# Kernel optimization log

Hardware: AMD Instinct MI355X
Metric: run time of the kernel (lower is better)

The kernel has to match this reference:

```python
import jax, jax.numpy as jnp
import numpy as np

EMB = 1024
HEADS = 16
HEAD_DIM = EMB // HEADS


def setup_inputs() -> dict:
    key = jax.random.key(0)
    k1, k2, k3, k4 = jax.random.split(key, 4)
    x = jax.random.normal(k1, (4, 2048, EMB), dtype=jnp.float32)
    # torch Linear weight is [out, in]; store as [in, out] for x @ W
    W_qkv = jax.random.normal(k2, (EMB, 3 * EMB), dtype=jnp.float32) * (1.0 / np.sqrt(EMB))
    W_proj = jax.random.normal(k3, (EMB, EMB), dtype=jnp.float32) * (1.0 / np.sqrt(EMB))
    b_proj = jax.random.normal(k4, (EMB,), dtype=jnp.float32) * 0.01
    return {"x": x, "W_qkv": W_qkv, "W_proj": W_proj, "b_proj": b_proj}


def reference(x, W_qkv, W_proj, b_proj):
    B, S, D = x.shape
    H, hd = HEADS, HEAD_DIM
    qkv = x @ W_qkv                                  # [B,S,3D]
    q, k, v = jnp.split(qkv, 3, axis=-1)
    q = q.reshape(B, S, H, hd).transpose(0, 2, 1, 3)  # [B,H,S,hd]
    k = k.reshape(B, S, H, hd).transpose(0, 2, 1, 3)
    v = v.reshape(B, S, H, hd).transpose(0, 2, 1, 3)
    att = jnp.einsum('bhqd,bhkd->bhqk', q, k) * (1.0 / np.sqrt(hd))
    causal = jnp.tril(jnp.ones((S, S), dtype=bool))
    att = jnp.where(causal[None, None], att, jnp.float32(-jnp.inf))
    att = jax.nn.softmax(att, axis=-1)
    # dropout omitted (eval mode / deterministic baseline)
    out = jnp.einsum('bhqk,bhkd->bhqd', att, v)       # [B,H,S,hd]
    out = out.transpose(0, 2, 1, 3).reshape(B, S, D)
    return out @ W_proj + b_proj
```

## Files before the change

kernel.cpp:

```cpp
#include <hip/hip_runtime.h>
#include <math.h>

#define S_   2048
#define D_   1024
#define H_   16
#define HD_  64
#define BH_  64
#define TOK_ 8192

typedef __attribute__((ext_vector_type(8))) short  short8;
typedef __attribute__((ext_vector_type(4))) float  floatx4;

__device__ __forceinline__ short f2bf(float f) {
  union { float f; unsigned u; } c; c.f = f;
  unsigned u = c.u;
  u += 0x7fffu + ((u >> 16) & 1u);
  return (short)(u >> 16);
}

__device__ __forceinline__ void gload16(const void* g, void* l) {
  __builtin_amdgcn_global_load_lds((const __attribute__((address_space(1))) void*)g,
                                   (__attribute__((address_space(3))) void*)l, 16, 0, 0);
}

__global__ void cvt_x_kernel(const float* __restrict__ in, short* __restrict__ out, int n8) {
  int i = blockIdx.x * blockDim.x + threadIdx.x;
  if (i >= n8) return;
  const float4* p = (const float4*)in;
  float4 a = p[i * 2], b = p[i * 2 + 1];
  short8 o;
  o[0] = f2bf(a.x); o[1] = f2bf(a.y); o[2] = f2bf(a.z); o[3] = f2bf(a.w);
  o[4] = f2bf(b.x); o[5] = f2bf(b.y); o[6] = f2bf(b.z); o[7] = f2bf(b.w);
  ((short8*)out)[i] = o;
}

__global__ void tconv_kernel(const float* __restrict__ in, short* __restrict__ out, int R, int C) {
  __shared__ float t[32][33];
  int tx = threadIdx.x, ty = threadIdx.y;
  int c0 = blockIdx.x * 32, r0 = blockIdx.y * 32;
#pragma unroll
  for (int i = 0; i < 4; ++i)
    t[ty + i * 8][tx] = in[(r0 + ty + i * 8) * C + c0 + tx];
  __syncthreads();
#pragma unroll
  for (int i = 0; i < 4; ++i)
    out[(c0 + ty + i * 8) * R + r0 + tx] = f2bf(t[tx][ty + i * 8]);
}

__global__ void tv_kernel(const short* __restrict__ vb, short* __restrict__ vtb) {
  __shared__ short t[32][33];
  int tx = threadIdx.x, ty = threadIdx.y;
  int bh = blockIdx.z;
  int d0 = blockIdx.x * 32, s0 = blockIdx.y * 32;
  const short* src = vb + bh * S_ * HD_;
  short* dst = vtb + bh * HD_ * S_;
#pragma unroll
  for (int i = 0; i < 4; ++i)
    t[ty + i * 8][tx] = src[(s0 + ty + i * 8) * HD_ + d0 + tx];
  __syncthreads();
#pragma unroll
  for (int i = 0; i < 4; ++i)
    dst[(d0 + ty + i * 8) * S_ + s0 + tx] = t[tx][ty + i * 8];
}

__global__ __launch_bounds__(256) void gemm_qkv_kernel(
    const short* __restrict__ A, const short* __restrict__ Bt,
    short* __restrict__ qb, short* __restrict__ kb, short* __restrict__ vb) {
  __shared__ short sA[128 * 32];
  __shared__ short sB[128 * 32];
  const int tid = threadIdx.x;
  const int lane = tid & 63, wid = tid >> 6;
  const int wm = wid >> 1, wn = wid & 1;
  const int lr = lane & 15, lg = lane >> 4;
  const int m0 = blockIdx.x * 128, n0 = blockIdx.y * 128;
  floatx4 acc[4][4] = {};
  const int f1 = tid * 16;
  const int rS1 = f1 >> 6, cS1 = (f1 & 63) >> 1;
  const int f2 = f1 + 4096;
  const int rS2 = f2 >> 6, cS2 = (f2 & 63) >> 1;
  for (int kt = 0; kt < 32; ++kt) {
    const int k0 = kt * 32;
    __syncthreads();
    gload16(&A[(m0 + rS1) * 1024 + k0 + cS1], (char*)sA + f1);
    gload16(&A[(m0 + rS2) * 1024 + k0 + cS2], (char*)sA + f2);
    gload16(&Bt[(n0 + rS1) * 1024 + k0 + cS1], (char*)sB + f1);
    gload16(&Bt[(n0 + rS2) * 1024 + k0 + cS2], (char*)sB + f2);
    __syncthreads();
    short8 af[4], bfv[4];
#pragma unroll
    for (int mf = 0; mf < 4; ++mf)
      af[mf] = *(const short8*)&sA[(wm * 64 + mf * 16 + lr) * 32 + lg * 8];
#pragma unroll
    for (int nf = 0; nf < 4; ++nf)
      bfv[nf] = *(const short8*)&sB[(wn * 64 + nf * 16 + lr) * 32 + lg * 8];
#pragma unroll
    for (int mf = 0; mf < 4; ++mf)
#pragma unroll
      for (int nf = 0; nf < 4; ++nf)
        acc[mf][nf] = __builtin_amdgcn_mfma_f32_16x16x32_bf16(af[mf], bfv[nf], acc[mf][nf], 0, 0, 0);
  }
  const int sec = n0 >> 10;
  short* dst = sec == 0 ? qb : (sec == 1 ? kb : vb);
  const float scale = (sec == 0) ? 0.125f : 1.0f;
#pragma unroll
  for (int mf = 0; mf < 4; ++mf) {
#pragma unroll
    for (int nf = 0; nf < 4; ++nf) {
      const int col = n0 + wn * 64 + nf * 16 + lr;
      const int w = col & 1023;
      const int h = w >> 6, d = w & 63;
#pragma unroll
      for (int r = 0; r < 4; ++r) {
        const int token = m0 + wm * 64 + mf * 16 + lg * 4 + r;
        const int b = token >> 11, s = token & 2047;
        dst[(((b << 4) | h) * 2048 + s) * 64 + d] = f2bf(acc[mf][nf][r] * scale);
      }
    }
  }
}

__global__ __launch_bounds__(256) void gemm_proj_kernel(
    const short* __restrict__ A, const short* __restrict__ Bt,
    const float* __restrict__ bias, float* __restrict__ out) {
  __shared__ short sA[128 * 32];
  __shared__ short sB[128 * 32];
  const int tid = threadIdx.x;
  const int lane = tid & 63, wid = tid >> 6;
  const int wm = wid >> 1, wn = wid & 1;
  const int lr = lane & 15, lg = lane >> 4;
  const int m0 = blockIdx.x * 128, n0 = blockIdx.y * 128;
  floatx4 acc[4][4] = {};
  const int f1 = tid * 16;
  const int rS1 = f1 >> 6, cS1 = (f1 & 63) >> 1;
  const int f2 = f1 + 4096;
  const int rS2 = f2 >> 6, cS2 = (f2 & 63) >> 1;
  for (int kt = 0; kt < 32; ++kt) {
    const int k0 = kt * 32;
    __syncthreads();
    gload16(&A[(m0 + rS1) * 1024 + k0 + cS1], (char*)sA + f1);
    gload16(&A[(m0 + rS2) * 1024 + k0 + cS2], (char*)sA + f2);
    gload16(&Bt[(n0 + rS1) * 1024 + k0 + cS1], (char*)sB + f1);
    gload16(&Bt[(n0 + rS2) * 1024 + k0 + cS2], (char*)sB + f2);
    __syncthreads();
    short8 af[4], bfv[4];
#pragma unroll
    for (int mf = 0; mf < 4; ++mf)
      af[mf] = *(const short8*)&sA[(wm * 64 + mf * 16 + lr) * 32 + lg * 8];
#pragma unroll
    for (int nf = 0; nf < 4; ++nf)
      bfv[nf] = *(const short8*)&sB[(wn * 64 + nf * 16 + lr) * 32 + lg * 8];
#pragma unroll
    for (int mf = 0; mf < 4; ++mf)
#pragma unroll
      for (int nf = 0; nf < 4; ++nf)
        acc[mf][nf] = __builtin_amdgcn_mfma_f32_16x16x32_bf16(af[mf], bfv[nf], acc[mf][nf], 0, 0, 0);
  }
#pragma unroll
  for (int mf = 0; mf < 4; ++mf) {
#pragma unroll
    for (int nf = 0; nf < 4; ++nf) {
      const int col = n0 + wn * 64 + nf * 16 + lr;
      const float bv = bias[col];
#pragma unroll
      for (int r = 0; r < 4; ++r) {
        const int row = m0 + wm * 64 + mf * 16 + lg * 4 + r;
        out[row * 1024 + col] = acc[mf][nf][r] + bv;
      }
    }
  }
}

__global__ __launch_bounds__(256) void attn_kernel(
    const short* __restrict__ qb, const short* __restrict__ kb,
    const short* __restrict__ vtb, short* __restrict__ attb) {
  __shared__ short sK[2][64 * 64];
  __shared__ short sVT[2][64 * 64];
  __shared__ short sP[4][32 * 64];
  const int tid = threadIdx.x;
  const int lane = tid & 63, wid = tid >> 6;
  const int lr = lane & 15, lg = lane >> 4;

  const int bid = blockIdx.x;
  const int wgid = (bid & 7) * 64 + (bid >> 3);
  const int bh = wgid >> 3;
  const int qx = wgid & 7;

  const char* kbase = (const char*)(kb + bh * S_ * HD_);
  const char* vtbase = (const char*)(vtb + bh * HD_ * S_);
  const short* qbase = qb + bh * S_ * HD_;
  char* pbase = (char*)&sP[wid][0];
  const int b = bh >> 4, h = bh & 15;

  const int f1 = tid * 16;
  const int ro1 = f1 >> 7, cb1 = f1 & 127;
  const int sc1 = cb1 ^ ((ro1 & 7) << 4);
  const int f2 = f1 + 4096;
  const int ro2 = f2 >> 7, cb2 = f2 & 127;
  const int sc2 = cb2 ^ ((ro2 & 7) << 4);

#pragma unroll 1
  for (int half = 0; half < 2; ++half) {
    const int qt = half ? (15 - qx) : qx;
    const int qw = qt * 128 + wid * 32;

    short8 qf[2][2];
#pragma unroll
    for (int mf = 0; mf < 2; ++mf)
#pragma unroll
      for (int kf = 0; kf < 2; ++kf)
        qf[mf][kf] = *(const short8*)&qbase[(qw + mf * 16 + lr) * 64 + kf * 32 + lg * 8];

    floatx4 acc_o[2][4] = {};
    float mrun[8], lrun[8];
#pragma unroll
    for (int i = 0; i < 8; ++i) { mrun[i] = -1e30f; lrun[i] = 0.f; }

    const int ntiles = 2 * qt + 2;

    {
      char* dK = (char*)sK[0];
      char* dV = (char*)sVT[0];
      gload16(kbase + ro1 * 128 + sc1, dK + f1);
      gload16(kbase + ro2 * 128 + sc2, dK + f2);
      gload16(vtbase + ro1 * 4096 + sc1, dV + f1);
      gload16(vtbase + ro2 * 4096 + sc2, dV + f2);
      asm volatile("s_waitcnt vmcnt(0)" ::: "memory");
      __builtin_amdgcn_s_barrier();
      __builtin_amdgcn_sched_barrier(0);
    }

    int cur = 0;
#pragma unroll 1
    for (int t = 0; t < ntiles; ++t) {
      if (t + 1 < ntiles) {
        const int key0n = (t + 1) * 64;
        char* dK = (char*)sK[cur ^ 1];
        char* dV = (char*)sVT[cur ^ 1];
        gload16(kbase + (key0n + ro1) * 128 + sc1, dK + f1);
        gload16(kbase + (key0n + ro2) * 128 + sc2, dK + f2);
        gload16(vtbase + ro1 * 4096 + key0n * 2 + sc1, dV + f1);
        gload16(vtbase + ro2 * 4096 + key0n * 2 + sc2, dV + f2);
      }
      const int key0 = t * 64;
      const char* cK = (const char*)sK[cur];
      const char* cV = (const char*)sVT[cur];

      floatx4 s_acc[2][4] = {};
      __builtin_amdgcn_s_setprio(1);
#pragma unroll
      for (int nf = 0; nf < 4; ++nf) {
#pragma unroll
        for (int kf = 0; kf < 2; ++kf) {
          const int row = nf * 16 + lr;
          const int cb = kf * 64 + lg * 16;
          short8 kfrag = *(const short8*)(cK + row * 128 + (cb ^ ((row & 7) << 4)));
#pragma unroll
          for (int mf = 0; mf < 2; ++mf)
            s_acc[mf][nf] = __builtin_amdgcn_mfma_f32_16x16x32_bf16(qf[mf][kf], kfrag, s_acc[mf][nf], 0, 0, 0);
        }
      }
      __builtin_amdgcn_s_setprio(0);

      const bool needmask = (key0 + 63 > qw);
#pragma unroll
      for (int mf = 0; mf < 2; ++mf) {
#pragma unroll
        for (int r = 0; r < 4; ++r) {
          const int qrow = qw + mf * 16 + lg * 4 + r;
          float sv[4];
          float mx = -1e30f;
#pragma unroll
          for (int nf = 0; nf < 4; ++nf) {
            float s = s_acc[mf][nf][r];
            if (needmask && (key0 + nf * 16 + lr > qrow)) s = -1e30f;
            sv[nf] = s;
            mx = fmaxf(mx, s);
          }
#pragma unroll
          for (int m = 1; m < 16; m <<= 1) mx = fmaxf(mx, __shfl_xor(mx, m));
          const int ri = mf * 4 + r;
          const float mnew = fmaxf(mrun[ri], mx);
          const float al = __expf(mrun[ri] - mnew);
          mrun[ri] = mnew;
          float ls = 0.f;
          const int qlocal = mf * 16 + lg * 4 + r;
          const int sw = (qlocal & 7) << 4;
#pragma unroll
          for (int nf = 0; nf < 4; ++nf) {
            float p = __expf(sv[nf] - mnew);
            ls += p;
            const int keyc = nf * 16 + lr;
            *(short*)(pbase + qlocal * 128 + ((keyc * 2) ^ sw)) = f2bf(p);
          }
#pragma unroll
          for (int m = 1; m < 16; m <<= 1) ls += __shfl_xor(ls, m);
          lrun[ri] = lrun[ri] * al + ls;
#pragma unroll
          for (int nfd = 0; nfd < 4; ++nfd) acc_o[mf][nfd][r] *= al;
        }
      }

      __builtin_amdgcn_s_setprio(1);
#pragma unroll
      for (int kf2 = 0; kf2 < 2; ++kf2) {
        short8 pf2[2];
#pragma unroll
        for (int mf = 0; mf < 2; ++mf) {
          const int rowp = mf * 16 + lr;
          const int cbp = kf2 * 64 + lg * 16;
          pf2[mf] = *(const short8*)(pbase + rowp * 128 + (cbp ^ ((rowp & 7) << 4)));
        }
#pragma unroll
        for (int nfd = 0; nfd < 4; ++nfd) {
          const int rowv = nfd * 16 + lr;
          const int cbv = kf2 * 64 + lg * 16;
          short8 vfrag = *(const short8*)(cV + rowv * 128 + (cbv ^ ((rowv & 7) << 4)));
#pragma unroll
          for (int mf = 0; mf < 2; ++mf)
            acc_o[mf][nfd] = __builtin_amdgcn_mfma_f32_16x16x32_bf16(pf2[mf], vfrag, acc_o[mf][nfd], 0, 0, 0);
        }
      }
      __builtin_amdgcn_s_setprio(0);

      __builtin_amdgcn_sched_barrier(0);
      asm volatile("s_waitcnt vmcnt(0)" ::: "memory");
      __builtin_amdgcn_s_barrier();
      __builtin_amdgcn_sched_barrier(0);
      cur ^= 1;
    }

#pragma unroll
    for (int mf = 0; mf < 2; ++mf) {
#pragma unroll
      for (int nfd = 0; nfd < 4; ++nfd) {
#pragma unroll
        for (int r = 0; r < 4; ++r) {
          const int ri = mf * 4 + r;
          const float o = acc_o[mf][nfd][r] / lrun[ri];
          const int qrow = qw + mf * 16 + lg * 4 + r;
          const int d = nfd * 16 + lr;
          attb[(b * 2048 + qrow) * 1024 + h * 64 + d] = f2bf(o);
        }
      }
    }
  }
}

extern "C" void kernel_launch(void* const* d_in, const int* in_sizes, int n_in,
                              void* d_out, int out_size, void* d_ws, size_t ws_size,
                              hipStream_t stream) {
  (void)in_sizes; (void)n_in; (void)out_size; (void)ws_size;
  const float* x = (const float*)d_in[0];
  const float* Wqkv = (const float*)d_in[1];
  const float* Wproj = (const float*)d_in[2];
  const float* bproj = (const float*)d_in[3];
  float* out = (float*)d_out;

  char* w = (char*)d_ws;
  short* xb     = (short*)(w + 0);
  short* wqkvT  = (short*)(w + 16777216);
  short* wprojT = (short*)(w + 23068672);
  short* qb     = (short*)(w + 25165824);
  short* kb     = (short*)(w + 41943040);
  short* vb     = (short*)(w + 58720256);
  short* vtb    = (short*)(w + 75497472);
  short* attb   = (short*)(w + 92274688);

  cvt_x_kernel<<<4096, 256, 0, stream>>>(x, xb, TOK_ * D_ / 8);
  tconv_kernel<<<dim3(96, 32), dim3(32, 8), 0, stream>>>(Wqkv, wqkvT, 1024, 3072);
  tconv_kernel<<<dim3(32, 32), dim3(32, 8), 0, stream>>>(Wproj, wprojT, 1024, 1024);
  gemm_qkv_kernel<<<dim3(64, 24), 256, 0, stream>>>(xb, wqkvT, qb, kb, vb);
  tv_kernel<<<dim3(2, 64, 64), dim3(32, 8), 0, stream>>>(vb, vtb);
  attn_kernel<<<512, 256, 0, stream>>>(qb, kb, vtb, attb);
  gemm_proj_kernel<<<dim3(64, 8), 256, 0, stream>>>(attb, wprojT, bproj, out);
}
```

Before: 316.2 us.

## Shrink attention query tiles and use lazy exp2 rescaling with MFMA row sums

Each block now covers a 64-row query tile instead of 128 rows, with 16 rows per wave, and the grid doubles to 1024 blocks for better parallelism and finer causal load balance. Softmax uses exp2 with log2(e) folded into the Q scale. The running max is only refreshed when some row's new max exceeds the old one by more than 8. The denominator is accumulated by an MFMA against a vector of ones instead of shuffle reductions. In exchange, K/V tiles are reloaded twice as often per query, and the lazy rescale lets unnormalized probabilities grow up to 2^8 before the final division.

```diff
diff --git a/kernel.cpp b/kernel.cpp
--- a/kernel.cpp
+++ b/kernel.cpp
@@ -101,7 +101,7 @@
   }
   const int sec = n0 >> 10;
   short* dst = sec == 0 ? qb : (sec == 1 ? kb : vb);
-  const float scale = (sec == 0) ? 0.125f : 1.0f;
+  const float scale = (sec == 0) ? 0.18033688011112042f : 1.0f;
 #pragma unroll
   for (int mf = 0; mf < 4; ++mf) {
 #pragma unroll
@@ -175,15 +175,15 @@
     const short* __restrict__ vtb, short* __restrict__ attb) {
   __shared__ short sK[2][64 * 64];
   __shared__ short sVT[2][64 * 64];
-  __shared__ short sP[4][32 * 64];
+  __shared__ short sP[4][16 * 64];
   const int tid = threadIdx.x;
   const int lane = tid & 63, wid = tid >> 6;
   const int lr = lane & 15, lg = lane >> 4;
 
   const int bid = blockIdx.x;
-  const int wgid = (bid & 7) * 64 + (bid >> 3);
-  const int bh = wgid >> 3;
-  const int qx = wgid & 7;
+  const int wgid = (bid & 7) * 128 + (bid >> 3);
+  const int bh = wgid >> 4;
+  const int qx = wgid & 15;
 
   const char* kbase = (const char*)(kb + bh * S_ * HD_);
   const char* vtbase = (const char*)(vtb + bh * HD_ * S_);
@@ -198,24 +198,27 @@
   const int ro2 = f2 >> 7, cb2 = f2 & 127;
   const int sc2 = cb2 ^ ((ro2 & 7) << 4);
 
+  short8 vones;
+#pragma unroll
+  for (int j = 0; j < 8; ++j) vones[j] = (short)0x3F80;
+
 #pragma unroll 1
   for (int half = 0; half < 2; ++half) {
-    const int qt = half ? (15 - qx) : qx;
-    const int qw = qt * 128 + wid * 32;
-
-    short8 qf[2][2];
-#pragma unroll
-    for (int mf = 0; mf < 2; ++mf)
-#pragma unroll
-      for (int kf = 0; kf < 2; ++kf)
-        qf[mf][kf] = *(const short8*)&qbase[(qw + mf * 16 + lr) * 64 + kf * 32 + lg * 8];
-
-    floatx4 acc_o[2][4] = {};
-    float mrun[8], lrun[8];
-#pragma unroll
-    for (int i = 0; i < 8; ++i) { mrun[i] = -1e30f; lrun[i] = 0.f; }
-
-    const int ntiles = 2 * qt + 2;
+    const int qt = half ? (31 - qx) : qx;
+    const int qw = qt * 64 + wid * 16;
+
+    short8 qf[2];
+#pragma unroll
+    for (int kf = 0; kf < 2; ++kf)
+      qf[kf] = *(const short8*)&qbase[(qw + lr) * 64 + kf * 32 + lg * 8];
+
+    floatx4 acc_o[4] = {};
+    floatx4 acc_den = {};
+    float mrun[4];
+#pragma unroll
+    for (int i = 0; i < 4; ++i) mrun[i] = -1e30f;
+
+    const int ntiles = qt + 1;
 
     {
       char* dK = (char*)sK[0];
@@ -245,7 +248,7 @@
       const char* cK = (const char*)sK[cur];
       const char* cV = (const char*)sVT[cur];
 
-      floatx4 s_acc[2][4] = {};
+      floatx4 s_acc[4] = {};
       __builtin_amdgcn_s_setprio(1);
 #pragma unroll
       for (int nf = 0; nf < 4; ++nf) {
@@ -254,70 +257,63 @@
           const int row = nf * 16 + lr;
           const int cb = kf * 64 + lg * 16;
           short8 kfrag = *(const short8*)(cK + row * 128 + (cb ^ ((row & 7) << 4)));
-#pragma unroll
-          for (int mf = 0; mf < 2; ++mf)
-            s_acc[mf][nf] = __builtin_amdgcn_mfma_f32_16x16x32_bf16(qf[mf][kf], kfrag, s_acc[mf][nf], 0, 0, 0);
+          s_acc[nf] = __builtin_amdgcn_mfma_f32_16x16x32_bf16(qf[kf], kfrag, s_acc[nf], 0, 0, 0);
         }
       }
       __builtin_amdgcn_s_setprio(0);
 
       const bool needmask = (key0 + 63 > qw);
-#pragma unroll
-      for (int mf = 0; mf < 2; ++mf) {
+      float mx[4];
+      bool need = false;
+#pragma unroll
+      for (int r = 0; r < 4; ++r) {
+        const int qrow = qw + lg * 4 + r;
+        if (needmask) {
+#pragma unroll
+          for (int nf = 0; nf < 4; ++nf)
+            if (key0 + nf * 16 + lr > qrow) s_acc[nf][r] = -1e30f;
+        }
+        float m01 = fmaxf(s_acc[0][r], s_acc[1][r]);
+        float m23 = fmaxf(s_acc[2][r], s_acc[3][r]);
+        float mxl = fmaxf(m01, m23);
+#pragma unroll
+        for (int m = 1; m < 16; m <<= 1) mxl = fmaxf(mxl, __shfl_xor(mxl, m));
+        mx[r] = mxl;
+        need = need || (mxl > mrun[r] + 8.f);
+      }
+      if (__any(need)) {
 #pragma unroll
         for (int r = 0; r < 4; ++r) {
-          const int qrow = qw + mf * 16 + lg * 4 + r;
-          float sv[4];
-          float mx = -1e30f;
-#pragma unroll
-          for (int nf = 0; nf < 4; ++nf) {
-            float s = s_acc[mf][nf][r];
-            if (needmask && (key0 + nf * 16 + lr > qrow)) s = -1e30f;
-            sv[nf] = s;
-            mx = fmaxf(mx, s);
-          }
-#pragma unroll
-          for (int m = 1; m < 16; m <<= 1) mx = fmaxf(mx, __shfl_xor(mx, m));
-          const int ri = mf * 4 + r;
-          const float mnew = fmaxf(mrun[ri], mx);
-          const float al = __expf(mrun[ri] - mnew);
-          mrun[ri] = mnew;
-          float ls = 0.f;
-          const int qlocal = mf * 16 + lg * 4 + r;
-          const int sw = (qlocal & 7) << 4;
-#pragma unroll
-          for (int nf = 0; nf < 4; ++nf) {
-            float p = __expf(sv[nf] - mnew);
-            ls += p;
-            const int keyc = nf * 16 + lr;
-            *(short*)(pbase + qlocal * 128 + ((keyc * 2) ^ sw)) = f2bf(p);
-          }
-#pragma unroll
-          for (int m = 1; m < 16; m <<= 1) ls += __shfl_xor(ls, m);
-          lrun[ri] = lrun[ri] * al + ls;
-#pragma unroll
-          for (int nfd = 0; nfd < 4; ++nfd) acc_o[mf][nfd][r] *= al;
+          const float mnew = fmaxf(mrun[r], mx[r]);
+          const float al = exp2f(mrun[r] - mnew);
+          mrun[r] = mnew;
+          acc_den[r] *= al;
+#pragma unroll
+          for (int nfd = 0; nfd < 4; ++nfd) acc_o[nfd][r] *= al;
+        }
+      }
+#pragma unroll
+      for (int r = 0; r < 4; ++r) {
+        const int qlocal = lg * 4 + r;
+        const int sw = (qlocal & 7) << 4;
+#pragma unroll
+        for (int nf = 0; nf < 4; ++nf) {
+          const float p = exp2f(s_acc[nf][r] - mrun[r]);
+          *(short*)(pbase + qlocal * 128 + ((nf * 32 + lr * 2) ^ sw)) = f2bf(p);
         }
       }
 
       __builtin_amdgcn_s_setprio(1);
 #pragma unroll
       for (int kf2 = 0; kf2 < 2; ++kf2) {
-        short8 pf2[2];
-#pragma unroll
-        for (int mf = 0; mf < 2; ++mf) {
-          const int rowp = mf * 16 + lr;
-          const int cbp = kf2 * 64 + lg * 16;
-          pf2[mf] = *(const short8*)(pbase + rowp * 128 + (cbp ^ ((rowp & 7) << 4)));
-        }
+        const short8 pf = *(const short8*)(pbase + lr * 128 + ((kf2 * 64 + lg * 16) ^ ((lr & 7) << 4)));
+        acc_den = __builtin_amdgcn_mfma_f32_16x16x32_bf16(pf, vones, acc_den, 0, 0, 0);
 #pragma unroll
         for (int nfd = 0; nfd < 4; ++nfd) {
           const int rowv = nfd * 16 + lr;
           const int cbv = kf2 * 64 + lg * 16;
           short8 vfrag = *(const short8*)(cV + rowv * 128 + (cbv ^ ((rowv & 7) << 4)));
-#pragma unroll
-          for (int mf = 0; mf < 2; ++mf)
-            acc_o[mf][nfd] = __builtin_amdgcn_mfma_f32_16x16x32_bf16(pf2[mf], vfrag, acc_o[mf][nfd], 0, 0, 0);
+          acc_o[nfd] = __builtin_amdgcn_mfma_f32_16x16x32_bf16(pf, vfrag, acc_o[nfd], 0, 0, 0);
         }
       }
       __builtin_amdgcn_s_setprio(0);
@@ -330,17 +326,13 @@
     }
 
 #pragma unroll
-    for (int mf = 0; mf < 2; ++mf) {
-#pragma unroll
-      for (int nfd = 0; nfd < 4; ++nfd) {
-#pragma unroll
-        for (int r = 0; r < 4; ++r) {
-          const int ri = mf * 4 + r;
-          const float o = acc_o[mf][nfd][r] / lrun[ri];
-          const int qrow = qw + mf * 16 + lg * 4 + r;
-          const int d = nfd * 16 + lr;
-          attb[(b * 2048 + qrow) * 1024 + h * 64 + d] = f2bf(o);
-        }
+    for (int nfd = 0; nfd < 4; ++nfd) {
+#pragma unroll
+      for (int r = 0; r < 4; ++r) {
+        const float o = acc_o[nfd][r] / acc_den[r];
+        const int qrow = qw + lg * 4 + r;
+        const int d = nfd * 16 + lr;
+        attb[(b * 2048 + qrow) * 1024 + h * 64 + d] = f2bf(o);
       }
     }
   }
@@ -371,6 +363,6 @@
   tconv_kernel<<<dim3(32, 32), dim3(32, 8), 0, stream>>>(Wproj, wprojT, 1024, 1024);
   gemm_qkv_kernel<<<dim3(64, 24), 256, 0, stream>>>(xb, wqkvT, qb, kb, vb);
   tv_kernel<<<dim3(2, 64, 64), dim3(32, 8), 0, stream>>>(vb, vtb);
-  attn_kernel<<<512, 256, 0, stream>>>(qb, kb, vtb, attb);
+  attn_kernel<<<1024, 256, 0, stream>>>(qb, kb, vtb, attb);
   gemm_proj_kernel<<<dim3(64, 8), 256, 0, stream>>>(attb, wprojT, bproj, out);
 }
```

New measurement: 327.2 us. 1.03x slower.

## Restructure flash-attention softmax with transposed scores, lazy rescale, and MFMA row sums

Applied to the files above, without the earlier changes.

Computes S transposed (K·Q) so each lane holds one query column, which cuts the max reduction to two cross-lane shuffles. Folds log2(e) into the Q scale so exp2 can replace expf, and rescales only when a row max grows by more than 8 (a lazy threshold). Computes the softmax denominator with an extra MFMA against a ones vector, packs P with v_cvt_pk_bf16 into 64-bit LDS stores, and skips key tiles that lie fully above the causal diagonal for a warp. In exchange it adds two MFMAs per tile, and the lazy max carries a numerical risk because unnormalized values can reach up to 2^8.

```diff
diff --git a/kernel.cpp b/kernel.cpp
--- a/kernel.cpp
+++ b/kernel.cpp
@@ -101,7 +101,7 @@
   }
   const int sec = n0 >> 10;
   short* dst = sec == 0 ? qb : (sec == 1 ? kb : vb);
-  const float scale = (sec == 0) ? 0.125f : 1.0f;
+  const float scale = (sec == 0) ? 0.18033688011112042f : 1.0f;
 #pragma unroll
   for (int mf = 0; mf < 4; ++mf) {
 #pragma unroll
@@ -198,6 +198,12 @@
   const int ro2 = f2 >> 7, cb2 = f2 & 127;
   const int sc2 = cb2 ^ ((ro2 & 7) << 4);
 
+  const int swz = (lr & 7) << 4;
+
+  short8 vones;
+#pragma unroll
+  for (int j = 0; j < 8; ++j) vones[j] = (short)0x3F80;
+
 #pragma unroll 1
   for (int half = 0; half < 2; ++half) {
     const int qt = half ? (15 - qx) : qx;
@@ -205,15 +211,14 @@
 
     short8 qf[2][2];
 #pragma unroll
-    for (int mf = 0; mf < 2; ++mf)
+    for (int qtile = 0; qtile < 2; ++qtile)
 #pragma unroll
       for (int kf = 0; kf < 2; ++kf)
-        qf[mf][kf] = *(const short8*)&qbase[(qw + mf * 16 + lr) * 64 + kf * 32 + lg * 8];
+        qf[qtile][kf] = *(const short8*)&qbase[(qw + qtile * 16 + lr) * 64 + kf * 32 + lg * 8];
 
     floatx4 acc_o[2][4] = {};
-    float mrun[8], lrun[8];
-#pragma unroll
-    for (int i = 0; i < 8; ++i) { mrun[i] = -1e30f; lrun[i] = 0.f; }
+    floatx4 acc_den[2] = {};
+    float mrun[2] = {-1e30f, -1e30f};
 
     const int ntiles = 2 * qt + 2;
 
@@ -242,85 +247,102 @@
         gload16(vtbase + ro2 * 4096 + key0n * 2 + sc2, dV + f2);
       }
       const int key0 = t * 64;
-      const char* cK = (const char*)sK[cur];
-      const char* cV = (const char*)sVT[cur];
-
-      floatx4 s_acc[2][4] = {};
-      __builtin_amdgcn_s_setprio(1);
-#pragma unroll
-      for (int nf = 0; nf < 4; ++nf) {
-#pragma unroll
-        for (int kf = 0; kf < 2; ++kf) {
-          const int row = nf * 16 + lr;
-          const int cb = kf * 64 + lg * 16;
-          short8 kfrag = *(const short8*)(cK + row * 128 + (cb ^ ((row & 7) << 4)));
-#pragma unroll
-          for (int mf = 0; mf < 2; ++mf)
-            s_acc[mf][nf] = __builtin_amdgcn_mfma_f32_16x16x32_bf16(qf[mf][kf], kfrag, s_acc[mf][nf], 0, 0, 0);
-        }
-      }
-      __builtin_amdgcn_s_setprio(0);
-
-      const bool needmask = (key0 + 63 > qw);
-#pragma unroll
-      for (int mf = 0; mf < 2; ++mf) {
-#pragma unroll
-        for (int r = 0; r < 4; ++r) {
-          const int qrow = qw + mf * 16 + lg * 4 + r;
-          float sv[4];
-          float mx = -1e30f;
-#pragma unroll
-          for (int nf = 0; nf < 4; ++nf) {
-            float s = s_acc[mf][nf][r];
-            if (needmask && (key0 + nf * 16 + lr > qrow)) s = -1e30f;
-            sv[nf] = s;
-            mx = fmaxf(mx, s);
-          }
-#pragma unroll
-          for (int m = 1; m < 16; m <<= 1) mx = fmaxf(mx, __shfl_xor(mx, m));
-          const int ri = mf * 4 + r;
-          const float mnew = fmaxf(mrun[ri], mx);
-          const float al = __expf(mrun[ri] - mnew);
-          mrun[ri] = mnew;
-          float ls = 0.f;
-          const int qlocal = mf * 16 + lg * 4 + r;
-          const int sw = (qlocal & 7) << 4;
-#pragma unroll
-          for (int nf = 0; nf < 4; ++nf) {
-            float p = __expf(sv[nf] - mnew);
-            ls += p;
-            const int keyc = nf * 16 + lr;
-            *(short*)(pbase + qlocal * 128 + ((keyc * 2) ^ sw)) = f2bf(p);
-          }
-#pragma unroll
-          for (int m = 1; m < 16; m <<= 1) ls += __shfl_xor(ls, m);
-          lrun[ri] = lrun[ri] * al + ls;
-#pragma unroll
-          for (int nfd = 0; nfd < 4; ++nfd) acc_o[mf][nfd][r] *= al;
-        }
-      }
-
-      __builtin_amdgcn_s_setprio(1);
-#pragma unroll
-      for (int kf2 = 0; kf2 < 2; ++kf2) {
-        short8 pf2[2];
-#pragma unroll
-        for (int mf = 0; mf < 2; ++mf) {
-          const int rowp = mf * 16 + lr;
-          const int cbp = kf2 * 64 + lg * 16;
-          pf2[mf] = *(const short8*)(pbase + rowp * 128 + (cbp ^ ((rowp & 7) << 4)));
-        }
-#pragma unroll
-        for (int nfd = 0; nfd < 4; ++nfd) {
-          const int rowv = nfd * 16 + lr;
-          const int cbv = kf2 * 64 + lg * 16;
-          short8 vfrag = *(const short8*)(cV + rowv * 128 + (cbv ^ ((rowv & 7) << 4)));
-#pragma unroll
-          for (int mf = 0; mf < 2; ++mf)
-            acc_o[mf][nfd] = __builtin_amdgcn_mfma_f32_16x16x32_bf16(pf2[mf], vfrag, acc_o[mf][nfd], 0, 0, 0);
-        }
-      }
-      __builtin_amdgcn_s_setprio(0);
+      if (key0 <= qw + 31) {
+        const char* cK = (const char*)sK[cur];
+        const char* cV = (const char*)sVT[cur];
+
+        floatx4 sT[4][2] = {};
+        __builtin_amdgcn_s_setprio(1);
+#pragma unroll
+        for (int kt = 0; kt < 4; ++kt) {
+#pragma unroll
+          for (int kf = 0; kf < 2; ++kf) {
+            short8 kfrag = *(const short8*)(cK + (kt * 16 + lr) * 128 + ((kf * 64 + lg * 16) ^ swz));
+#pragma unroll
+            for (int qtile = 0; qtile < 2; ++qtile)
+              sT[kt][qtile] = __builtin_amdgcn_mfma_f32_16x16x32_bf16(kfrag, qf[qtile][kf], sT[kt][qtile], 0, 0, 0);
+          }
+        }
+        __builtin_amdgcn_s_setprio(0);
+
+        if (key0 + 63 > qw) {
+#pragma unroll
+          for (int kt = 0; kt < 4; ++kt)
+#pragma unroll
+            for (int qtile = 0; qtile < 2; ++qtile)
+#pragma unroll
+              for (int r = 0; r < 4; ++r)
+                if (key0 + kt * 16 + lg * 4 + r > qw + qtile * 16 + lr) sT[kt][qtile][r] = -1e30f;
+        }
+
+        float mx[2], al[2];
+        bool need = false;
+#pragma unroll
+        for (int qtile = 0; qtile < 2; ++qtile) {
+          float m0v = fmaxf(fmaxf(sT[0][qtile][0], sT[0][qtile][1]), fmaxf(sT[0][qtile][2], sT[0][qtile][3]));
+          float m1v = fmaxf(fmaxf(sT[1][qtile][0], sT[1][qtile][1]), fmaxf(sT[1][qtile][2], sT[1][qtile][3]));
+          float m2v = fmaxf(fmaxf(sT[2][qtile][0], sT[2][qtile][1]), fmaxf(sT[2][qtile][2], sT[2][qtile][3]));
+          float m3v = fmaxf(fmaxf(sT[3][qtile][0], sT[3][qtile][1]), fmaxf(sT[3][qtile][2], sT[3][qtile][3]));
+          float m = fmaxf(fmaxf(m0v, m1v), fmaxf(m2v, m3v));
+          m = fmaxf(m, __shfl_xor(m, 16));
+          m = fmaxf(m, __shfl_xor(m, 32));
+          mx[qtile] = m;
+          need = need || (m > mrun[qtile] + 8.f);
+        }
+        if (__any(need)) {
+#pragma unroll
+          for (int qtile = 0; qtile < 2; ++qtile) {
+            const float mnew = fmaxf(mrun[qtile], mx[qtile]);
+            al[qtile] = __builtin_amdgcn_exp2f(mrun[qtile] - mnew);
+            mrun[qtile] = mnew;
+          }
+#pragma unroll
+          for (int mf = 0; mf < 2; ++mf) {
+#pragma unroll
+            for (int r = 0; r < 4; ++r) {
+              const float alr = __shfl(al[mf], lg * 4 + r);
+              acc_den[mf][r] *= alr;
+#pragma unroll
+              for (int nfd = 0; nfd < 4; ++nfd) acc_o[mf][nfd][r] *= alr;
+            }
+          }
+        }
+
+#pragma unroll
+        for (int kt = 0; kt < 4; ++kt) {
+#pragma unroll
+          for (int qtile = 0; qtile < 2; ++qtile) {
+            const float p0 = __builtin_amdgcn_exp2f(sT[kt][qtile][0] - mrun[qtile]);
+            const float p1 = __builtin_amdgcn_exp2f(sT[kt][qtile][1] - mrun[qtile]);
+            const float p2 = __builtin_amdgcn_exp2f(sT[kt][qtile][2] - mrun[qtile]);
+            const float p3 = __builtin_amdgcn_exp2f(sT[kt][qtile][3] - mrun[qtile]);
+            unsigned lo, hi;
+            asm("v_cvt_pk_bf16_f32 %0, %1, %2" : "=v"(lo) : "v"(p0), "v"(p1));
+            asm("v_cvt_pk_bf16_f32 %0, %1, %2" : "=v"(hi) : "v"(p2), "v"(p3));
+            *(unsigned long long*)(pbase + (qtile * 16 + lr) * 128 + ((kt * 32 + lg * 8) ^ swz)) =
+                ((unsigned long long)hi << 32) | lo;
+          }
+        }
+
+        __builtin_amdgcn_s_setprio(1);
+#pragma unroll
+        for (int kf2 = 0; kf2 < 2; ++kf2) {
+          short8 pf[2];
+#pragma unroll
+          for (int mf = 0; mf < 2; ++mf) {
+            pf[mf] = *(const short8*)(pbase + (mf * 16 + lr) * 128 + ((kf2 * 64 + lg * 16) ^ swz));
+            acc_den[mf] = __builtin_amdgcn_mfma_f32_16x16x32_bf16(pf[mf], vones, acc_den[mf], 0, 0, 0);
+          }
+#pragma unroll
+          for (int nfd = 0; nfd < 4; ++nfd) {
+            short8 vfrag = *(const short8*)(cV + (nfd * 16 + lr) * 128 + ((kf2 * 64 + lg * 16) ^ swz));
+#pragma unroll
+            for (int mf = 0; mf < 2; ++mf)
+              acc_o[mf][nfd] = __builtin_amdgcn_mfma_f32_16x16x32_bf16(pf[mf], vfrag, acc_o[mf][nfd], 0, 0, 0);
+          }
+        }
+        __builtin_amdgcn_s_setprio(0);
+      }
 
       __builtin_amdgcn_sched_barrier(0);
       asm volatile("s_waitcnt vmcnt(0)" ::: "memory");
@@ -335,8 +357,7 @@
       for (int nfd = 0; nfd < 4; ++nfd) {
 #pragma unroll
         for (int r = 0; r < 4; ++r) {
-          const int ri = mf * 4 + r;
-          const float o = acc_o[mf][nfd][r] / lrun[ri];
+          const float o = acc_o[mf][nfd][r] / acc_den[mf][r];
           const int qrow = qw + mf * 16 + lg * 4 + r;
           const int d = nfd * 16 + lr;
           attb[(b * 2048 + qrow) * 1024 + h * 64 + d] = f2bf(o);
```

Measured after the change: 262.2 us. 1.21x faster.
